# Kernel optimization log

Hardware: AMD Instinct MI355X
Metric: run time of the kernel (lower is better)

The kernel has to match this reference:

```python
import jax, jax.numpy as jnp
import numpy as np
from jax import lax

# ---- static config (ProposalLayer config object) ----
BASE_SIZE = 16
RATIOS = np.array([0.5, 1.0, 2.0])
SCALES = np.array([8.0, 16.0, 32.0])
STRIDE = 16
PRE_NMS_TOPN = 6000
POST_NMS_TOPN = 300
MIN_THRESHOLD = 16.0
NMS_THRESH = 0.7
IMG_W = 4096
IMG_H = 2048
NEG_INF = jnp.float32(-1e30)


def _generate_anchors(base_size, ratios, scales):
    w = h = float(base_size)
    x_ctr = y_ctr = 0.5 * (base_size - 1)
    size = w * h
    size_ratios = size / ratios
    ws = np.round(np.sqrt(size_ratios))          # (R,)
    hs = np.round(ws * ratios)                   # (R,)
    ws = (ws[:, None] * scales[None, :]).ravel() # (R*S,)
    hs = (hs[:, None] * scales[None, :]).ravel()
    anchors = np.stack([x_ctr - 0.5 * (ws - 1), y_ctr - 0.5 * (hs - 1),
                        x_ctr + 0.5 * (ws - 1), y_ctr + 0.5 * (hs - 1)], axis=1)
    return anchors.astype(np.float32)            # (A, 4) in x1,y1,x2,y2


def _all_anchors(height, width, stride):
    anchors = _generate_anchors(BASE_SIZE, RATIOS, SCALES)      # (A,4)
    sx = np.arange(width) * stride
    sy = np.arange(height) * stride
    mx, my = np.meshgrid(sx, sy)                                # (H,W) each
    shifts = np.stack([mx.ravel(), my.ravel(), mx.ravel(), my.ravel()], axis=1)
    shifts = shifts.reshape(-1, 1, 4).astype(np.float32)        # (K,1,4), K iterates h-major
    return (anchors[None] + shifts).reshape(-1, 4)              # (K*A, 4)


def _decode(deltas, anchors):
    # deltas: (B, N, 4); anchors: (N, 4) -> boxes (B, N, 4)
    aw = anchors[:, 2] - anchors[:, 0] + 1.0
    ah = anchors[:, 3] - anchors[:, 1] + 1.0
    acx = anchors[:, 0] + 0.5 * (aw - 1.0)
    acy = anchors[:, 1] + 0.5 * (ah - 1.0)
    dx, dy, dw, dh = deltas[..., 0], deltas[..., 1], deltas[..., 2], deltas[..., 3]
    pcx = dx * aw + acx
    pcy = dy * ah + acy
    pw = jnp.exp(dw) * aw
    ph = jnp.exp(dh) * ah
    return jnp.stack([pcx - 0.5 * pw, pcy - 0.5 * ph,
                      pcx + 0.5 * pw, pcy + 0.5 * ph], axis=-1)


def _nms_single(boxes, scores):
    # boxes (N,4), scores (N,) -> greedy NMS, fixed POST_NMS_TOPN outputs
    areas = (boxes[:, 2] - boxes[:, 0] + 1.0) * (boxes[:, 3] - boxes[:, 1] + 1.0)

    def body(live, _):
        i = jnp.argmax(live)
        box = boxes[i]
        sc = scores[i]
        xx1 = jnp.maximum(box[0], boxes[:, 0])
        yy1 = jnp.maximum(box[1], boxes[:, 1])
        xx2 = jnp.minimum(box[2], boxes[:, 2])
        yy2 = jnp.minimum(box[3], boxes[:, 3])
        inter = jnp.maximum(xx2 - xx1 + 1.0, 0.0) * jnp.maximum(yy2 - yy1 + 1.0, 0.0)
        iou = inter / (areas[i] + areas - inter)
        live = jnp.where(iou > NMS_THRESH, NEG_INF, live)
        live = live.at[i].set(NEG_INF)
        return live, (box, sc)

    _, (out_boxes, out_scores) = lax.scan(body, scores, None, length=POST_NMS_TOPN)
    return out_boxes, out_scores  # (P,4), (P,)


def reference(labels_pred, bbox_reg):
    B = labels_pred.shape[0]
    H, W = labels_pred.shape[-2:]
    anchors = jnp.asarray(_all_anchors(H, W, STRIDE))           # (K*A,4)

    # objectness score = fg channel after (B,2A,H,W)->(B,H,W,2A)->(B,KA,2)
    scores = jnp.transpose(labels_pred, (0, 2, 3, 1)).reshape(B, -1, 2)[..., 1]
    deltas = jnp.transpose(bbox_reg, (0, 2, 3, 1)).reshape(B, -1, 4)

    boxes = _decode(deltas, anchors)                            # (B,KA,4)
    x = jnp.clip(boxes[..., 0::2], 0.0, IMG_W - 1.0)
    y = jnp.clip(boxes[..., 1::2], 0.0, IMG_H - 1.0)
    boxes = jnp.stack([x[..., 0], y[..., 0], x[..., 1], y[..., 1]], axis=-1)

    keep = ((boxes[..., 2] - boxes[..., 0] + 1.0 >= MIN_THRESHOLD) &
            (boxes[..., 3] - boxes[..., 1] + 1.0 >= MIN_THRESHOLD))
    masked = jnp.where(keep, scores, NEG_INF)

    # pre-NMS top-k of kept anchors by score (assumes keep.sum >= PRE_NMS_TOPN)
    top_scores_masked, idx = lax.top_k(masked, PRE_NMS_TOPN)    # (B,P)
    top_scores = jnp.take_along_axis(scores, idx, axis=1)
    top_boxes = jnp.take_along_axis(boxes, idx[..., None], axis=1)

    out_boxes, out_scores = jax.vmap(_nms_single)(top_boxes, top_scores)
    return out_boxes, out_scores


def setup_inputs() -> dict:
    key = jax.random.key(0)
    k1, k2 = jax.random.split(key)
    labels_pred = jax.random.normal(k1, (16, 18, 128, 256), dtype=jnp.float32)
    bbox_reg = jax.random.normal(k2, (16, 36, 128, 256), dtype=jnp.float32)
    return {"labels_pred": labels_pred, "bbox_reg": bbox_reg}
```

## Files before the change

kernel.cpp:

```cpp
#include <hip/hip_runtime.h>
#include <stdint.h>

#define NBATCH 16
#define NANCH  9
#define NHGT   128
#define NWID   256
#define NHW    (NHGT * NWID)
#define NTOT   (NHW * NANCH)
#define PRE    6000
#define POST   300
#define CAPN   8192
#define BINS   8192
#define BIN_SHIFT 19
#define NWORDS 94
#define RROWS  384
#define SWORDS 6

#define MIDP 0x1.6666668p-1

__device__ __constant__ float c_AW[NANCH] = {184.f,368.f,736.f,128.f,256.f,512.f,88.f,176.f,352.f};
__device__ __constant__ float c_AH[NANCH] = {96.f,192.f,384.f,128.f,256.f,512.f,176.f,352.f,704.f};

__device__ __forceinline__ uint32_t f2key(float f) {
    uint32_t u = __float_as_uint(f);
    return (u & 0x80000000u) ? ~u : (u | 0x80000000u);
}

__device__ __forceinline__ bool iou_sup(const float4 bi, float areaI, const float4 bj, float areaJ) {
    float xx1 = fmaxf(bi.x, bj.x);
    float yy1 = fmaxf(bi.y, bj.y);
    float xx2 = fminf(bi.z, bj.z);
    float yy2 = fminf(bi.w, bj.w);
    float iw = fmaxf(__fadd_rn(__fsub_rn(xx2, xx1), 1.f), 0.f);
    float ih = fmaxf(__fadd_rn(__fsub_rn(yy2, yy1), 1.f), 0.f);
    float inter = __fmul_rn(iw, ih);
    float uni = __fsub_rn(__fadd_rn(areaI, areaJ), inter);
    return ((double)inter >= (double)uni * MIDP);
}

__device__ __forceinline__ bool decode_clip(float dx, float dy, float dw, float dh,
                                            float aw, float ah, float acx, float acy,
                                            float& x1, float& y1, float& x2, float& y2) {
    float pcx = __fadd_rn(__fmul_rn(dx, aw), acx);
    float pcy = __fadd_rn(__fmul_rn(dy, ah), acy);
    float pw  = __fmul_rn(expf(dw), aw);
    float ph  = __fmul_rn(expf(dh), ah);
    float hx  = __fmul_rn(0.5f, pw);
    float hy  = __fmul_rn(0.5f, ph);
    x1 = __fsub_rn(pcx, hx);
    y1 = __fsub_rn(pcy, hy);
    x2 = __fadd_rn(pcx, hx);
    y2 = __fadd_rn(pcy, hy);
    x1 = fminf(fmaxf(x1, 0.f), 4095.f);
    x2 = fminf(fmaxf(x2, 0.f), 4095.f);
    y1 = fminf(fmaxf(y1, 0.f), 2047.f);
    y2 = fminf(fmaxf(y2, 0.f), 2047.f);
    float wpl = __fadd_rn(__fsub_rn(x2, x1), 1.f);
    float hpl = __fadd_rn(__fsub_rn(y2, y1), 1.f);
    return (wpl >= 16.f) && (hpl >= 16.f);
}

__global__ __launch_bounds__(256) void k_zero(uint4* __restrict__ ghist4) {
    ghist4[blockIdx.x * 256 + threadIdx.x] = make_uint4(0, 0, 0, 0);
}

__global__ __launch_bounds__(256) void k_hist(const float* __restrict__ lab,
                                              const float* __restrict__ reg,
                                              uint32_t* __restrict__ ghist,
                                              uint32_t* __restrict__ keys) {
    __shared__ uint32_t hist[BINS];
    for (int i = threadIdx.x; i < BINS; i += 256) hist[i] = 0;
    __syncthreads();
    int b = blockIdx.x >> 5, sub = blockIdx.x & 31;
    int hw = (sub << 10) | (threadIdx.x << 2);
    int h = hw >> 8, w = hw & 255;
    const float* lb = lab + (size_t)b * 18 * NHW + hw;
    const float* rb = reg + (size_t)b * 36 * NHW + hw;
    uint32_t* kb = keys + (size_t)b * NANCH * NHW + hw;
    float acy  = (float)(h * 16) + 7.5f;
    float acx0 = (float)(w * 16) + 7.5f;
    float acx1 = acx0 + 16.0f;
    float acx2 = acx0 + 32.0f;
    float acx3 = acx0 + 48.0f;
#pragma unroll
    for (int a = 0; a < NANCH; ++a) {
        float4 s  = *(const float4*)&lb[(2 * a + 1) * NHW];
        float4 dx = *(const float4*)&rb[(4 * a + 0) * NHW];
        float4 dy = *(const float4*)&rb[(4 * a + 1) * NHW];
        float4 dwv = *(const float4*)&rb[(4 * a + 2) * NHW];
        float4 dhv = *(const float4*)&rb[(4 * a + 3) * NHW];
        float x1, y1, x2, y2;
        bool k0 = decode_clip(dx.x, dy.x, dwv.x, dhv.x, c_AW[a], c_AH[a], acx0, acy, x1, y1, x2, y2);
        bool k1 = decode_clip(dx.y, dy.y, dwv.y, dhv.y, c_AW[a], c_AH[a], acx1, acy, x1, y1, x2, y2);
        bool k2 = decode_clip(dx.z, dy.z, dwv.z, dhv.z, c_AW[a], c_AH[a], acx2, acy, x1, y1, x2, y2);
        bool k3 = decode_clip(dx.w, dy.w, dwv.w, dhv.w, c_AW[a], c_AH[a], acx3, acy, x1, y1, x2, y2);
        uint32_t key0 = f2key(k0 ? s.x : -1e30f);
        uint32_t key1 = f2key(k1 ? s.y : -1e30f);
        uint32_t key2 = f2key(k2 ? s.z : -1e30f);
        uint32_t key3 = f2key(k3 ? s.w : -1e30f);
        *(uint4*)&kb[a * NHW] = make_uint4(key0, key1, key2, key3);
        atomicAdd(&hist[key0 >> BIN_SHIFT], 1u);
        atomicAdd(&hist[key1 >> BIN_SHIFT], 1u);
        atomicAdd(&hist[key2 >> BIN_SHIFT], 1u);
        atomicAdd(&hist[key3 >> BIN_SHIFT], 1u);
    }
    __syncthreads();
    uint32_t* gh = ghist + ((size_t)b << 13);
    for (int i = threadIdx.x; i < BINS; i += 256) {
        uint32_t c = hist[i];
        if (c) atomicAdd(&gh[i], c);
    }
}

__global__ __launch_bounds__(256) void k_thresh(const uint32_t* __restrict__ ghist,
                                                uint32_t* __restrict__ thresh,
                                                uint32_t* __restrict__ cnt) {
    __shared__ uint32_t part[256];
    int b = blockIdx.x;
    const uint32_t* gh = ghist + ((size_t)b << 13);
    uint32_t p = 0;
    int base = threadIdx.x * 32;
    for (int k = 0; k < 32; ++k) p += gh[base + k];
    part[threadIdx.x] = p;
    __syncthreads();
    if (threadIdx.x == 0) {
        uint32_t cum = 0;
        int tb = 0;
        for (int c = 255; c >= 0; --c) {
            if (cum + part[c] >= (uint32_t)PRE) {
                for (int i = 31; i >= 0; --i) {
                    cum += gh[c * 32 + i];
                    if (cum >= (uint32_t)PRE) { tb = c * 32 + i; break; }
                }
                break;
            }
            cum += part[c];
        }
        thresh[b] = (uint32_t)tb << BIN_SHIFT;
        cnt[b] = 0;
    }
}

__global__ __launch_bounds__(256) void k_compact(const uint32_t* __restrict__ keys,
                                                 const uint32_t* __restrict__ thresh,
                                                 uint32_t* __restrict__ cnt,
                                                 uint64_t* __restrict__ cand) {
    __shared__ uint64_t stage[2304];
    __shared__ uint32_t sCount;
    __shared__ uint32_t sBase;
    if (threadIdx.x == 0) sCount = 0;
    __syncthreads();
    int bid = blockIdx.x;
    int b = bid >> 7;
    int hw = ((bid & 127) << 8) | threadIdx.x;
    int lane = threadIdx.x & 63;
    const uint32_t* kb = keys + (size_t)b * NANCH * NHW + hw;
    uint32_t th = thresh[b];
#pragma unroll
    for (int a = 0; a < NANCH; ++a) {
        uint32_t key = kb[a * NHW];
        bool valid = (key >= th);
        uint64_t mask = __ballot(valid);
        if (mask) {
            int leader = __ffsll((unsigned long long)mask) - 1;
            uint32_t wb = 0;
            if (lane == leader) wb = atomicAdd(&sCount, (uint32_t)__popcll(mask));
            wb = (uint32_t)__shfl((int)wb, leader);
            if (valid) {
                int rank = __popcll(mask & ((1ull << lane) - 1ull));
                uint32_t n = (uint32_t)(hw * NANCH + a);
                stage[wb + rank] = ((uint64_t)key << 32) | (uint32_t)(~n);
            }
        }
    }
    __syncthreads();
    if (threadIdx.x == 0) sBase = atomicAdd(&cnt[b], sCount);
    __syncthreads();
    uint32_t total = sCount, base = sBase;
    for (uint32_t i = threadIdx.x; i < total; i += 256) {
        uint32_t pos = base + i;
        if (pos < (uint32_t)CAPN) cand[(size_t)b * CAPN + pos] = stage[i];
    }
}

__global__ __launch_bounds__(512) void k_sortA(const uint32_t* __restrict__ cnt,
                                               uint64_t* __restrict__ cand) {
    __shared__ uint64_t sm[1024];
    int b = blockIdx.x >> 3, c = blockIdx.x & 7;
    uint32_t C = cnt[b];
    if (C > (uint32_t)CAPN) C = CAPN;
    uint64_t* cb = cand + (size_t)b * CAPN;
    int base = c << 10;
    for (int li = threadIdx.x; li < 1024; li += 512) {
        int gi = base + li;
        sm[li] = (gi < (int)C) ? cb[gi] : 0ull;
    }
    __syncthreads();
    for (int k = 2; k <= 1024; k <<= 1) {
        for (int j = k >> 1; j > 0; j >>= 1) {
            for (int li = threadIdx.x; li < 1024; li += 512) {
                int lxj = li ^ j;
                if (lxj > li) {
                    uint64_t va = sm[li], vb = sm[lxj];
                    bool up = ((li & k) == 0);
                    bool sw = up ? (va < vb) : (va > vb);
                    if (sw) { sm[li] = vb; sm[lxj] = va; }
                }
            }
            __syncthreads();
        }
    }
    for (int li = threadIdx.x; li < 1024; li += 512) cb[base + li] = sm[li];
}

__global__ __launch_bounds__(256) void k_merge(const uint64_t* __restrict__ src,
                                               uint64_t* __restrict__ dst,
                                               int Rlog) {
    int g = blockIdx.x * 256 + threadIdx.x;
    if (g >= NBATCH * CAPN) return;
    int b = g >> 13;
    int p = g & (CAPN - 1);
    int R = 1 << Rlog;
    int pair = p >> (Rlog + 1);
    int q = p & ((R << 1) - 1);
    const uint64_t* A = src + (size_t)b * CAPN + ((size_t)(pair << 1) << Rlog);
    const uint64_t* B = A + R;
    int lo = (q > R) ? (q - R) : 0;
    int hi = (q < R) ? q : R;
    while (lo < hi) {
        int mid = (lo + hi) >> 1;
        if (A[mid] > B[q - mid - 1]) lo = mid + 1; else hi = mid;
    }
    int i = lo, j = q - lo;
    uint64_t aV = (i < R) ? A[i] : 0ull;
    uint64_t bV = (j < R) ? B[j] : 0ull;
    dst[(size_t)b * CAPN + p] = (aV > bV) ? aV : bV;
}

__global__ __launch_bounds__(256) void k_mergegather(const uint64_t* __restrict__ cand,
                                                     const float* __restrict__ lab,
                                                     const float* __restrict__ reg,
                                                     float4* __restrict__ boxes,
                                                     float* __restrict__ scores) {
    int g = blockIdx.x * 256 + threadIdx.x;
    if (g >= NBATCH * PRE) return;
    int b = g / PRE, p = g - b * PRE;
    const uint64_t* A = cand + (size_t)b * CAPN;
    const uint64_t* B = A + 4096;
    int lo = (p > 4096) ? (p - 4096) : 0;
    int hi = (p < 4096) ? p : 4096;
    while (lo < hi) {
        int mid = (lo + hi) >> 1;
        if (A[mid] > B[p - mid - 1]) lo = mid + 1; else hi = mid;
    }
    int i = lo, j = p - lo;
    uint64_t aV = (i < 4096) ? A[i] : 0ull;
    uint64_t bV = (j < 4096) ? B[j] : 0ull;
    uint64_t v = (aV > bV) ? aV : bV;
    uint32_t n = ~(uint32_t)(v & 0xFFFFFFFFull);
    if (n >= (uint32_t)NTOT) n = 0;
    int a = (int)(n % NANCH);
    int hw = (int)(n / NANCH);
    int w = hw & 255, h = hw >> 8;
    const float* lb0 = lab + (size_t)b * 18 * NHW;
    const float* rb0 = reg + (size_t)b * 36 * NHW;
    float s  = lb0[(2 * a + 1) * NHW + hw];
    float dx = rb0[(4 * a + 0) * NHW + hw];
    float dy = rb0[(4 * a + 1) * NHW + hw];
    float dwv = rb0[(4 * a + 2) * NHW + hw];
    float dhv = rb0[(4 * a + 3) * NHW + hw];
    float acx = (float)(w * 16) + 7.5f;
    float acy = (float)(h * 16) + 7.5f;
    float x1, y1, x2, y2;
    decode_clip(dx, dy, dwv, dhv, c_AW[a], c_AH[a], acx, acy, x1, y1, x2, y2);
    boxes[b * PRE + p] = make_float4(x1, y1, x2, y2);
    scores[b * PRE + p] = s;
}

__global__ __launch_bounds__(512) void k_iou(const float4* __restrict__ boxes,
                                             uint64_t* __restrict__ supp) {
    __shared__ float4 lb[RROWS];
    __shared__ float  la[RROWS];
    int blk = blockIdx.x % 48;
    int b   = blockIdx.x / 48;
    const float4* bb = boxes + b * PRE;
    for (int i = threadIdx.x; i < RROWS; i += 512) {
        float4 v = bb[i];
        lb[i] = v;
        la[i] = __fmul_rn(__fadd_rn(__fsub_rn(v.z, v.x), 1.f),
                          __fadd_rn(__fsub_rn(v.w, v.y), 1.f));
    }
    __syncthreads();
    int wave = threadIdx.x >> 6, lane = threadIdx.x & 63;
    int r = (blk << 3) + wave;
    float4 bi = lb[r];
    float ai = la[r];
    uint64_t* sr = supp + ((size_t)b * RROWS + r) * SWORDS;
#pragma unroll
    for (int w = 0; w < SWORDS; ++w) {
        int j = (w << 6) | lane;
        bool s = iou_sup(bi, ai, lb[j], la[j]);
        uint64_t m = __ballot(s);
        if (lane == 0) sr[w] = m;
    }
}

#define RD32(V, L) __builtin_amdgcn_readlane((uint32_t)(V), (L))
#define RDL64(V, L) ((uint64_t)(uint32_t)RD32((V), (L)) | \
                     ((uint64_t)(uint32_t)RD32((uint32_t)((V) >> 32), (L)) << 32))

#define LOADW(I) do {                                                           \
    const uint64_t* _rp = sbase + (size_t)(((I) << 6) + lane) * SWORDS;         \
    m##I##0 = _rp[0]; m##I##1 = _rp[1]; m##I##2 = _rp[2];                       \
    m##I##3 = _rp[3]; m##I##4 = _rp[4]; m##I##5 = _rp[5];                       \
} while (0)

#define WINDOW(I) {                                                             \
    uint64_t curw = s##I;                                                       \
    while (curw) {                                                              \
        int rl = __ffsll((unsigned long long)curw) - 1;                         \
        if (lane == 0) sidx[t] = (uint32_t)(((I) << 6) + rl);                   \
        ++t;                                                                    \
        s0 &= ~RDL64(m##I##0, rl); s1 &= ~RDL64(m##I##1, rl);                   \
        s2 &= ~RDL64(m##I##2, rl); s3 &= ~RDL64(m##I##3, rl);                   \
        s4 &= ~RDL64(m##I##4, rl); s5 &= ~RDL64(m##I##5, rl);                   \
        if (t >= POST) goto walk_done;                                          \
        curw = s##I;                                                            \
    }                                                                           \
}

__global__ __launch_bounds__(64, 1) void k_walk(const uint64_t* __restrict__ supp,
                                                const float4* __restrict__ boxes,
                                                const float* __restrict__ scores,
                                                uint32_t* __restrict__ flags,
                                                float* __restrict__ out) {
    __shared__ uint32_t sidx[POST];
    int b = blockIdx.x;
    int lane = threadIdx.x;
    const uint64_t* sbase = supp + (size_t)b * RROWS * SWORDS;
    uint64_t m00,m01,m02,m03,m04,m05;
    uint64_t m10,m11,m12,m13,m14,m15;
    uint64_t m20,m21,m22,m23,m24,m25;
    uint64_t m30,m31,m32,m33,m34,m35;
    uint64_t m40,m41,m42,m43,m44,m45;
    uint64_t m50,m51,m52,m53,m54,m55;
    LOADW(0); LOADW(1); LOADW(2); LOADW(3); LOADW(4); LOADW(5);
    uint64_t s0 = ~0ull, s1 = ~0ull, s2 = ~0ull, s3 = ~0ull, s4 = ~0ull, s5 = ~0ull;
    int t = 0;
    WINDOW(0)
    WINDOW(1)
    WINDOW(2)
    WINDOW(3)
    WINDOW(4)
    WINDOW(5)
    if (lane == 0) flags[b] = 1u;
    return;
walk_done:
    __syncthreads();
    for (int tt = lane; tt < POST; tt += 64) {
        uint32_t i = sidx[tt];
        float4 bc = boxes[b * PRE + i];
        size_t ob = ((size_t)b * POST + tt) * 4;
        out[ob + 0] = bc.x; out[ob + 1] = bc.y;
        out[ob + 2] = bc.z; out[ob + 3] = bc.w;
        out[(size_t)NBATCH * POST * 4 + (size_t)b * POST + tt] = scores[b * PRE + i];
    }
    if (lane == 0) flags[b] = 0u;
}

__global__ __launch_bounds__(512) void k_resume(const float4* __restrict__ boxes,
                                                const float* __restrict__ scores,
                                                const uint32_t* __restrict__ flags,
                                                float* __restrict__ out) {
    int b = blockIdx.x;
    if (flags[b] == 0) return;
    __shared__ uint64_t alive[NWORDS];
    __shared__ uint32_t sCur;
    int tid = threadIdx.x;
    const float4* bb = boxes + b * PRE;
    const float* sb = scores + b * PRE;
    if (tid < NWORDS) alive[tid] = (tid == NWORDS - 1) ? ((1ull << 48) - 1ull) : ~0ull;
    __syncthreads();
    for (int t = 0; t < POST; ++t) {
        if (tid == 0) sCur = 0xFFFFFFFFu;
        __syncthreads();
        if (tid < NWORDS) {
            uint64_t wd = alive[tid];
            if (wd) atomicMin(&sCur, (uint32_t)(tid * 64 + (__ffsll((unsigned long long)wd) - 1)));
        }
        __syncthreads();
        uint32_t cur = sCur;
        uint32_t e = (cur < (uint32_t)PRE) ? cur : 0u;
        float4 bc = bb[e];
        if (tid == 0) {
            size_t ob = ((size_t)b * POST + t) * 4;
            out[ob + 0] = bc.x; out[ob + 1] = bc.y;
            out[ob + 2] = bc.z; out[ob + 3] = bc.w;
            out[(size_t)NBATCH * POST * 4 + (size_t)b * POST + t] = sb[e];
            if (cur < (uint32_t)PRE)
                atomicAnd(&alive[cur >> 6], ~(1ull << (cur & 63)));
        }
        if (cur < (uint32_t)PRE) {
            float areaC = __fmul_rn(__fadd_rn(__fsub_rn(bc.z, bc.x), 1.f),
                                    __fadd_rn(__fsub_rn(bc.w, bc.y), 1.f));
            for (uint32_t j = cur + 1 + tid; j < (uint32_t)PRE; j += 512) {
                uint64_t wd = alive[j >> 6];
                if ((wd >> (j & 63)) & 1ull) {
                    float4 bj = bb[j];
                    float areaJ = __fmul_rn(__fadd_rn(__fsub_rn(bj.z, bj.x), 1.f),
                                            __fadd_rn(__fsub_rn(bj.w, bj.y), 1.f));
                    if (iou_sup(bc, areaC, bj, areaJ))
                        atomicAnd(&alive[j >> 6], ~(1ull << (j & 63)));
                }
            }
        }
        __syncthreads();
    }
}

extern "C" void kernel_launch(void* const* d_in, const int* in_sizes, int n_in,
                              void* d_out, int out_size, void* d_ws, size_t ws_size,
                              hipStream_t stream) {
    (void)in_sizes; (void)n_in; (void)out_size; (void)ws_size;
    const float* lab = (const float*)d_in[0];
    const float* reg = (const float*)d_in[1];
    float* out = (float*)d_out;
    char* ws = (char*)d_ws;

    uint32_t* ghist  = (uint32_t*)(ws + 0);
    uint32_t* cnt    = (uint32_t*)(ws + 524288);
    uint32_t* thr    = (uint32_t*)(ws + 524352);
    uint64_t* cand   = (uint64_t*)(ws + 524416);
    float4*   boxes  = (float4*)  (ws + 1572992);
    float*    scores = (float*)   (ws + 3108992);
    uint64_t* supp   = (uint64_t*)(ws + 3492992);
    uint32_t* flags  = (uint32_t*)(ws + 3787904);
    uint32_t* keys   = (uint32_t*)(ws + 3787968);
    uint64_t* cand2  = (uint64_t*)(ws + 22662336);

    k_zero       <<<128, 256, 0, stream>>>((uint4*)ghist);
    k_hist       <<<512, 256, 0, stream>>>(lab, reg, ghist, keys);
    k_thresh     <<<NBATCH, 256, 0, stream>>>(ghist, thr, cnt);
    k_compact    <<<2048, 256, 0, stream>>>(keys, thr, cnt, cand);
    k_sortA      <<<NBATCH * 8, 512, 0, stream>>>(cnt, cand);
    k_merge      <<<NBATCH * CAPN / 256, 256, 0, stream>>>(cand, cand2, 10);
    k_merge      <<<NBATCH * CAPN / 256, 256, 0, stream>>>(cand2, cand, 11);
    k_mergegather<<<(NBATCH * PRE + 255) / 256, 256, 0, stream>>>(cand, lab, reg, boxes, scores);
    k_iou        <<<NBATCH * 48, 512, 0, stream>>>(boxes, supp);
    k_walk       <<<NBATCH, 64, 0, stream>>>(supp, boxes, scores, flags, out);
    k_resume     <<<NBATCH, 512, 0, stream>>>(boxes, scores, flags, out);
}
```

Before: 151.0 us.

## Sort 2048-element chunks to drop a merge pass and fuse walk with resume

The block-local bitonic sort now handles 2048 elements per block with 1024 threads instead of 1024 elements with 512 threads. This removes one global merge-pass launch, so the merge-gather stage reads from cand2. The NMS bitmask walk and the fallback resume kernel are merged into one 512-thread kernel that communicates through shared memory instead of a global flags array. This cuts two kernel launches and one full pass over the candidate buffer, at the cost of a longer in-block sort with more barrier steps and a larger block for the walk.

Measured after the change: 153.6 us. No clear change (+1.7%).

```diff
diff --git a/kernel.cpp b/kernel.cpp
--- a/kernel.cpp
+++ b/kernel.cpp
@@ -183,22 +183,22 @@
     }
 }
 
-__global__ __launch_bounds__(512) void k_sortA(const uint32_t* __restrict__ cnt,
-                                               uint64_t* __restrict__ cand) {
-    __shared__ uint64_t sm[1024];
-    int b = blockIdx.x >> 3, c = blockIdx.x & 7;
+__global__ __launch_bounds__(1024) void k_sortB(const uint32_t* __restrict__ cnt,
+                                                uint64_t* __restrict__ cand) {
+    __shared__ uint64_t sm[2048];
+    int b = blockIdx.x >> 2, c = blockIdx.x & 3;
     uint32_t C = cnt[b];
     if (C > (uint32_t)CAPN) C = CAPN;
     uint64_t* cb = cand + (size_t)b * CAPN;
-    int base = c << 10;
-    for (int li = threadIdx.x; li < 1024; li += 512) {
+    int base = c << 11;
+    for (int li = threadIdx.x; li < 2048; li += 1024) {
         int gi = base + li;
         sm[li] = (gi < (int)C) ? cb[gi] : 0ull;
     }
     __syncthreads();
-    for (int k = 2; k <= 1024; k <<= 1) {
+    for (int k = 2; k <= 2048; k <<= 1) {
         for (int j = k >> 1; j > 0; j >>= 1) {
-            for (int li = threadIdx.x; li < 1024; li += 512) {
+            for (int li = threadIdx.x; li < 2048; li += 1024) {
                 int lxj = li ^ j;
                 if (lxj > li) {
                     uint64_t va = sm[li], vb = sm[lxj];
@@ -210,7 +210,7 @@
             __syncthreads();
         }
     }
-    for (int li = threadIdx.x; li < 1024; li += 512) cb[base + li] = sm[li];
+    for (int li = threadIdx.x; li < 2048; li += 1024) cb[base + li] = sm[li];
 }
 
 __global__ __launch_bounds__(256) void k_merge(const uint64_t* __restrict__ src,
@@ -329,56 +329,55 @@
     }                                                                           \
 }
 
-__global__ __launch_bounds__(64, 1) void k_walk(const uint64_t* __restrict__ supp,
-                                                const float4* __restrict__ boxes,
-                                                const float* __restrict__ scores,
-                                                uint32_t* __restrict__ flags,
-                                                float* __restrict__ out) {
+__global__ __launch_bounds__(512, 1) void k_walkres(const uint64_t* __restrict__ supp,
+                                                    const float4* __restrict__ boxes,
+                                                    const float* __restrict__ scores,
+                                                    float* __restrict__ out) {
     __shared__ uint32_t sidx[POST];
-    int b = blockIdx.x;
-    int lane = threadIdx.x;
-    const uint64_t* sbase = supp + (size_t)b * RROWS * SWORDS;
-    uint64_t m00,m01,m02,m03,m04,m05;
-    uint64_t m10,m11,m12,m13,m14,m15;
-    uint64_t m20,m21,m22,m23,m24,m25;
-    uint64_t m30,m31,m32,m33,m34,m35;
-    uint64_t m40,m41,m42,m43,m44,m45;
-    uint64_t m50,m51,m52,m53,m54,m55;
-    LOADW(0); LOADW(1); LOADW(2); LOADW(3); LOADW(4); LOADW(5);
-    uint64_t s0 = ~0ull, s1 = ~0ull, s2 = ~0ull, s3 = ~0ull, s4 = ~0ull, s5 = ~0ull;
-    int t = 0;
-    WINDOW(0)
-    WINDOW(1)
-    WINDOW(2)
-    WINDOW(3)
-    WINDOW(4)
-    WINDOW(5)
-    if (lane == 0) flags[b] = 1u;
-    return;
-walk_done:
-    __syncthreads();
-    for (int tt = lane; tt < POST; tt += 64) {
-        uint32_t i = sidx[tt];
-        float4 bc = boxes[b * PRE + i];
-        size_t ob = ((size_t)b * POST + tt) * 4;
-        out[ob + 0] = bc.x; out[ob + 1] = bc.y;
-        out[ob + 2] = bc.z; out[ob + 3] = bc.w;
-        out[(size_t)NBATCH * POST * 4 + (size_t)b * POST + tt] = scores[b * PRE + i];
-    }
-    if (lane == 0) flags[b] = 0u;
-}
-
-__global__ __launch_bounds__(512) void k_resume(const float4* __restrict__ boxes,
-                                                const float* __restrict__ scores,
-                                                const uint32_t* __restrict__ flags,
-                                                float* __restrict__ out) {
-    int b = blockIdx.x;
-    if (flags[b] == 0) return;
+    __shared__ uint32_t sFlag;
     __shared__ uint64_t alive[NWORDS];
     __shared__ uint32_t sCur;
+    int b = blockIdx.x;
     int tid = threadIdx.x;
     const float4* bb = boxes + b * PRE;
     const float* sb = scores + b * PRE;
+    if (tid < 512 && tid >= 64) {
+    } else if (tid < 64) {
+        int lane = tid;
+        const uint64_t* sbase = supp + (size_t)b * RROWS * SWORDS;
+        uint64_t m00,m01,m02,m03,m04,m05;
+        uint64_t m10,m11,m12,m13,m14,m15;
+        uint64_t m20,m21,m22,m23,m24,m25;
+        uint64_t m30,m31,m32,m33,m34,m35;
+        uint64_t m40,m41,m42,m43,m44,m45;
+        uint64_t m50,m51,m52,m53,m54,m55;
+        LOADW(0); LOADW(1); LOADW(2); LOADW(3); LOADW(4); LOADW(5);
+        uint64_t s0 = ~0ull, s1 = ~0ull, s2 = ~0ull, s3 = ~0ull, s4 = ~0ull, s5 = ~0ull;
+        int t = 0;
+        WINDOW(0)
+        WINDOW(1)
+        WINDOW(2)
+        WINDOW(3)
+        WINDOW(4)
+        WINDOW(5)
+        if (lane == 0) sFlag = 1u;
+        goto walk_exit;
+walk_done:
+        if (lane == 0) sFlag = 0u;
+walk_exit: ;
+    }
+    __syncthreads();
+    if (sFlag == 0u) {
+        for (int tt = tid; tt < POST; tt += 512) {
+            uint32_t i = sidx[tt];
+            float4 bc = bb[i];
+            size_t ob = ((size_t)b * POST + tt) * 4;
+            out[ob + 0] = bc.x; out[ob + 1] = bc.y;
+            out[ob + 2] = bc.z; out[ob + 3] = bc.w;
+            out[(size_t)NBATCH * POST * 4 + (size_t)b * POST + tt] = sb[i];
+        }
+        return;
+    }
     if (tid < NWORDS) alive[tid] = (tid == NWORDS - 1) ? ((1ull << 48) - 1ull) : ~0ull;
     __syncthreads();
     for (int t = 0; t < POST; ++t) {
@@ -434,19 +433,16 @@
     float4*   boxes  = (float4*)  (ws + 1572992);
     float*    scores = (float*)   (ws + 3108992);
     uint64_t* supp   = (uint64_t*)(ws + 3492992);
-    uint32_t* flags  = (uint32_t*)(ws + 3787904);
-    uint32_t* keys   = (uint32_t*)(ws + 3787968);
-    uint64_t* cand2  = (uint64_t*)(ws + 22662336);
+    uint32_t* keys   = (uint32_t*)(ws + 3787904);
+    uint64_t* cand2  = (uint64_t*)(ws + 22662272);
 
     k_zero       <<<128, 256, 0, stream>>>((uint4*)ghist);
     k_hist       <<<512, 256, 0, stream>>>(lab, reg, ghist, keys);
     k_thresh     <<<NBATCH, 256, 0, stream>>>(ghist, thr, cnt);
     k_compact    <<<2048, 256, 0, stream>>>(keys, thr, cnt, cand);
-    k_sortA      <<<NBATCH * 8, 512, 0, stream>>>(cnt, cand);
-    k_merge      <<<NBATCH * CAPN / 256, 256, 0, stream>>>(cand, cand2, 10);
-    k_merge      <<<NBATCH * CAPN / 256, 256, 0, stream>>>(cand2, cand, 11);
-    k_mergegather<<<(NBATCH * PRE + 255) / 256, 256, 0, stream>>>(cand, lab, reg, boxes, scores);
+    k_sortB      <<<NBATCH * 4, 1024, 0, stream>>>(cnt, cand);
+    k_merge      <<<NBATCH * CAPN / 256, 256, 0, stream>>>(cand, cand2, 11);
+    k_mergegather<<<(NBATCH * PRE + 255) / 256, 256, 0, stream>>>(cand2, lab, reg, boxes, scores);
     k_iou        <<<NBATCH * 48, 512, 0, stream>>>(boxes, supp);
-    k_walk       <<<NBATCH, 64, 0, stream>>>(supp, boxes, scores, flags, out);
-    k_resume     <<<NBATCH, 512, 0, stream>>>(boxes, scores, flags, out);
-}
+    k_walkres    <<<NBATCH, 512, 0, stream>>>(supp, boxes, scores, out);
+}
```
